# Kernel tuning notes

Measured on AMD Instinct MI355X. Metric: run time of the kernel, lower is better.

The kernel has to match this reference:

```python
import jax, jax.numpy as jnp
import numpy as np

B, N, T, F_IN, H, OUT = 64, 207, 48, 6, 64, 1
RANK = 24  # fixed inner dim of learned adjacency factors


def setup_inputs() -> dict:
    key = jax.random.key(0)
    ks = jax.random.split(key, 10)
    s = lambda k, shp, sc=1.0: jax.random.normal(k, shp, jnp.float32) * sc
    return {
        "x": s(ks[0], (B, N, T, F_IN)),
        "N1": s(ks[1], (N, RANK)),
        "N2": s(ks[2], (RANK, N)),
        "W1": s(ks[3], (F_IN, H), 0.2),
        "b1": jnp.zeros((H,), jnp.float32),
        "W2": s(ks[4], (H, H), 0.1),
        "b2": jnp.zeros((H,), jnp.float32),
        "W_ih": s(ks[5], (4 * H, H), 0.1),
        "W_hh": s(ks[6], (4 * H, H), 0.1),
        "b_ih": jnp.zeros((4 * H,), jnp.float32),
        "b_hh": jnp.zeros((4 * H,), jnp.float32),
        "W_fc": s(ks[7], (H, OUT), 0.1),
        "b_fc": jnp.zeros((OUT,), jnp.float32),
    }


def reference(x, N1, N2, W1, b1, W2, b2, W_ih, W_hh, b_ih, b_hh, W_fc, b_fc):
    Bn, Nn, Tn, Fn = x.shape
    # sigmoid(N1@N2) > 0 everywhere -> dense_to_sparse yields ALL N^2 edges
    # (self-loops included); GCNConv's gcn_norm adds one extra self-loop,
    # edge weights all 1 -> A = ones + I, deg = N+1, symmetric normalization.
    adj = jax.nn.sigmoid(N1 @ N2)
    mask = (adj > 0).astype(x.dtype)  # structurally all-ones
    A = mask + jnp.eye(Nn, dtype=x.dtype)
    dinv = jax.lax.rsqrt(A.sum(axis=1))
    A_hat = dinv[:, None] * A * dinv[None, :]  # [N, N]

    xt = jnp.transpose(x, (0, 2, 1, 3))  # [B, T, N, F]
    # GCNConv: propagate(x @ W) with sym-norm, then bias; relu; dropout=eval no-op
    h = jax.nn.relu(jnp.einsum('mn,btnh->btmh', A_hat, xt @ W1) + b1)
    h = jax.nn.relu(jnp.einsum('mn,btnh->btmh', A_hat, h @ W2) + b2)

    # [B, T, N, H] -> [B*N, T, H] for the LSTM
    seq = jnp.transpose(h, (0, 2, 1, 3)).reshape(Bn * Nn, Tn, -1)
    Hd = W_hh.shape[1]

    def step(carry, x_t):
        h_prev, c_prev = carry
        g = x_t @ W_ih.T + b_ih + h_prev @ W_hh.T + b_hh
        i, f, gg, o = jnp.split(g, 4, axis=-1)  # torch gate order i,f,g,o
        c = jax.nn.sigmoid(f) * c_prev + jax.nn.sigmoid(i) * jnp.tanh(gg)
        h_new = jax.nn.sigmoid(o) * jnp.tanh(c)
        return (h_new, c), None

    h0 = jnp.zeros((Bn * Nn, Hd), x.dtype)
    (hT, _), _ = jax.lax.scan(step, (h0, h0), jnp.transpose(seq, (1, 0, 2)))
    out = hT @ W_fc + b_fc  # [B*N, OUT]
    return out.reshape(Bn, Nn, -1)
```

## Files before the change

kernel.cpp:

```cpp
#include <hip/hip_runtime.h>
#include <math.h>

#define NB 64
#define NN 207
#define NT 48
#define NF 6
#define NH 64
#define NSEQ (NB*NN)
#define NG   (NSEQ/16)
#define TSTRIDE ((size_t)NSEQ*NH)

typedef short bf8_t __attribute__((ext_vector_type(8)));
typedef float f4_t  __attribute__((ext_vector_type(4)));
typedef unsigned short ushort;
typedef unsigned int uint;

__device__ __forceinline__ ushort bf16h(float x){
  uint u = __float_as_uint(x);
  return (ushort)((u + 0x7FFF + ((u>>16)&1)) >> 16);
}
__device__ __forceinline__ float bf16f(ushort h){
  return __uint_as_float((uint)h << 16);
}
__device__ __forceinline__ float fsig(float x){
  return __builtin_amdgcn_rcpf(1.0f + __expf(-x));
}
__device__ __forceinline__ float ftanh(float x){
  x = fminf(15.0f, fmaxf(-15.0f, x));
  float e = __expf(2.0f*x);
  return 1.0f - 2.0f*__builtin_amdgcn_rcpf(e + 1.0f);
}


#define HW 72
#define XS4 28
#define GCN6_LDS_BYTES (208*HW*2 + (207*XS4 + NF*64 + 64 + 64 + 256 + 256 + 32)*4)

__global__ __launch_bounds__(256, 2) void gcn_kernel(
    const float* __restrict__ x, const float* __restrict__ W1, const float* __restrict__ b1,
    const float* __restrict__ W2, const float* __restrict__ b2, uint* __restrict__ sxp)
{
  extern __shared__ char smraw[];
  ushort* h1b = (ushort*)smraw;
  float*  xs4 = (float*)(h1b + 208*HW);
  float*  W1s = xs4 + 207*XS4;
  float*  b1s = W1s + NF*64;
  float*  b2s = b1s + 64;
  float*  S2_ = b2s + 64;
  float*  r1_ = S2_ + 256;
  float*  xsA = r1_ + 256;

  const int tid = threadIdx.x;
  const int tg = blockIdx.x, b = blockIdx.y;
  const float inv = 1.0f/208.0f;
  const int l = tid & 63;
  const int w = __builtin_amdgcn_readfirstlane(tid >> 6);
  const int col = l & 15, q = l >> 4;
  const int cw = w*16 + col;

  S2_[tid] = 0.f;
  r1_[tid] = 0.f;
  if (tid < 32) xsA[tid] = 0.f;
  if (tid < 72) h1b[207*HW + tid] = 0;

  for (int i=tid;i<NF*64;i+=256) W1s[i]=W1[i];
  if (tid<64){ b1s[tid]=b1[tid]; b2s[tid]=b2[tid]; }
  {
    const float* xb = x + (size_t)b*NN*(NT*NF) + (size_t)tg*24;
    for (int i=tid; i<207*6; i+=256){
      int n = i/6, c = (i - n*6)*4;
      *(float4*)&xs4[n*XS4 + c] = *(const float4*)&xb[(size_t)n*(NT*NF) + c];
    }
  }
  __syncthreads();

  if (tid < 192){
    int tt = tid/48, rem = tid - tt*48, f = rem>>3, p = rem&7;
    float ps = 0.f;
    for (int n=p; n<NN; n+=8) ps += xs4[n*XS4 + tt*6 + f];
    atomicAdd(&xsA[tt*8+f], ps);
  }

  float wtmp[16];
  #pragma unroll
  for (int kc=0;kc<2;kc++)
    #pragma unroll
    for (int j=0;j<8;j++)
      wtmp[kc*8+j] = W2[(size_t)(kc*32 + q*8 + j)*64 + cw];
  bf8_t B2[2];
  #pragma unroll
  for (int kc=0;kc<2;kc++){
    bf8_t ph;
    #pragma unroll
    for (int j=0;j<8;j++) ph[j] = (short)bf16h(wtmp[kc*8+j]);
    B2[kc]=ph;
  }
  __syncthreads();

  const int ht4 = (tid & 15) * 4;
  const int nti = tid >> 4;

  #pragma unroll 1
  for (int tt=0; tt<4; tt++){
    const int t = tg*4 + tt;
    {
      float s1v[4];
      #pragma unroll
      for (int j=0;j<4;j++){
        float a = 0.f;
        #pragma unroll
        for (int f=0;f<NF;f++) a += xsA[tt*8+f]*W1s[f*64 + ht4 + j];
        s1v[j] = a;
      }
      float cs0=0.f, cs1=0.f, cs2=0.f, cs3=0.f;
      #pragma unroll 1
      for (int p=0;p<4;p++){
        int nt = p*16 + nti;
        if (nt < 52){
          #pragma unroll
          for (int i=0;i<4;i++){
            int n = 4*nt+i;
            if (n < NN){
              float a0=0.f,a1=0.f,a2=0.f,a3=0.f;
              #pragma unroll
              for (int f=0;f<NF;f++){
                float xv = xs4[n*XS4 + tt*6 + f];
                float4 wv = *(const float4*)&W1s[f*64 + ht4];
                a0+=xv*wv.x; a1+=xv*wv.y; a2+=xv*wv.z; a3+=xv*wv.w;
              }
              float v0=(a0+s1v[0])*inv + b1s[ht4+0]; v0 = v0>0.f?v0:0.f;
              float v1=(a1+s1v[1])*inv + b1s[ht4+1]; v1 = v1>0.f?v1:0.f;
              float v2=(a2+s1v[2])*inv + b1s[ht4+2]; v2 = v2>0.f?v2:0.f;
              float v3=(a3+s1v[3])*inv + b1s[ht4+3]; v3 = v3>0.f?v3:0.f;
              ushort4 hi;
              hi.x=bf16h(v0); hi.y=bf16h(v1); hi.z=bf16h(v2); hi.w=bf16h(v3);
              *(ushort4*)&h1b[n*HW + ht4] = hi;
              cs0+=v0; cs1+=v1; cs2+=v2; cs3+=v3;
            }
          }
        }
      }
      atomicAdd(&r1_[tt*64+ht4+0], cs0);
      atomicAdd(&r1_[tt*64+ht4+1], cs1);
      atomicAdd(&r1_[tt*64+ht4+2], cs2);
      atomicAdd(&r1_[tt*64+ht4+3], cs3);
    }
    __syncthreads();

    {
      int h = tid & 63, pp = tid >> 6;
      float ps = 0.f;
      #pragma unroll
      for (int k=0;k<16;k++) ps += r1_[tt*64+pp*16+k]*W2[(size_t)(pp*16+k)*64 + h];
      atomicAdd(&S2_[tt*64+h], ps);
    }

    f4_t acc[13];
    #pragma unroll
    for (int mt=0;mt<13;mt++){ f4_t z; z[0]=0.f;z[1]=0.f;z[2]=0.f;z[3]=0.f; acc[mt]=z; }
    #pragma unroll 2
    for (int mt=0;mt<13;mt++){
      #pragma unroll
      for (int kc=0;kc<2;kc++){
        bf8_t ah = *(const bf8_t*)(h1b + (mt*16+col)*HW + kc*32 + q*8);
        acc[mt] = __builtin_amdgcn_mfma_f32_16x16x32_bf16(ah, B2[kc], acc[mt], 0,0,0);
      }
    }
    __syncthreads();

    {
      const float s2v = S2_[tt*64+cw], b2v = b2s[cw];
      uint* obase = sxp + ((size_t)t*NSEQ + (size_t)b*NN)*NH + cw;
      #pragma unroll
      for (int mt=0;mt<13;mt++){
        #pragma unroll
        for (int r=0;r<4;r++){
          int n = mt*16 + q*4 + r;
          if (n < NN){
            float v = (acc[mt][r] + s2v)*inv + b2v;
            v = v>0.f ? v : 0.f;
            ushort hb = bf16h(v);
            ushort lb = bf16h(v - bf16f(hb));
            obase[(size_t)n*NH] = ((uint)hb<<16) | (uint)lb;
          }
        }
      }
    }
  }
}

#define HS 68

__global__ __launch_bounds__(256, 1) void lstm8_kernel(
    const uint* __restrict__ sxp,
    const float* __restrict__ Wih, const float* __restrict__ Whh,
    const float* __restrict__ bih, const float* __restrict__ bhh,
    const float* __restrict__ Wfc, const float* __restrict__ bfc, float* __restrict__ out)
{
  __shared__ uint hf[2][16*HS + 4];

  const int tid = threadIdx.x;
  const int l = tid & 63;
  const int w = __builtin_amdgcn_readfirstlane(tid >> 6);
  const int col = l & 15, q = l >> 4;
  const int g = blockIdx.x;

  bf8_t Bh[4][4], Bl[4][4];
  #pragma unroll
  for (int mat=0; mat<2; mat++){
    const float* W = mat ? Whh : Wih;
    #pragma unroll
    for (int ty=0; ty<4; ty++){
      #pragma unroll
      for (int kk=0; kk<2; kk++){
        const float* wp = W + (size_t)(ty*64 + w*16 + col)*64 + kk*32 + q*8;
        bf8_t ph, pl;
        #pragma unroll
        for (int j=0;j<8;j++){
          float wv = wp[j];
          ushort hb = bf16h(wv);
          ph[j] = (short)hb;
          pl[j] = (short)bf16h(wv - bf16f(hb));
        }
        Bh[ty][mat*2+kk] = ph;
        Bl[ty][mat*2+kk] = pl;
      }
    }
  }
  float bias[4];
  #pragma unroll
  for (int ty=0;ty<4;ty++){
    int r = ty*64 + w*16 + col;
    bias[ty] = bih[r] + bhh[r];
  }
  float c[4];
  #pragma unroll
  for (int i=0;i<4;i++) c[i]=0.f;

  for (int i=tid; i<16*HS; i+=256) hf[0][i] = 0;

  const uint* xg = sxp + (size_t)g*1024 + (size_t)(col*64 + q*8);
  uint4 cA0, cA1, cB0, cB1;
  cA0 = *(const uint4*)(xg);
  cA1 = *(const uint4*)(xg + 4);
  cB0 = *(const uint4*)(xg + 32);
  cB1 = *(const uint4*)(xg + 36);

  const int d = w*16 + col;
  const uint* hrd = &hf[0][0] + col*HS + q*8;
  __syncthreads();

  #pragma unroll 2
  for (int t=0; t<NT; t++){
    const int cur = t & 1;
    bf8_t xh[2], xl[2];
    {
      uint u[8];
      u[0]=cA0.x;u[1]=cA0.y;u[2]=cA0.z;u[3]=cA0.w;u[4]=cA1.x;u[5]=cA1.y;u[6]=cA1.z;u[7]=cA1.w;
      #pragma unroll
      for (int j=0;j<8;j++){ xh[0][j]=(short)(u[j]>>16); xl[0][j]=(short)(u[j]&0xffff); }
      u[0]=cB0.x;u[1]=cB0.y;u[2]=cB0.z;u[3]=cB0.w;u[4]=cB1.x;u[5]=cB1.y;u[6]=cB1.z;u[7]=cB1.w;
      #pragma unroll
      for (int j=0;j<8;j++){ xh[1][j]=(short)(u[j]>>16); xl[1][j]=(short)(u[j]&0xffff); }
    }
    if (t+1 < NT){
      const uint* xn = xg + (size_t)(t+1)*TSTRIDE;
      cA0 = *(const uint4*)(xn);
      cA1 = *(const uint4*)(xn + 4);
      cB0 = *(const uint4*)(xn + 32);
      cB1 = *(const uint4*)(xn + 36);
    }
    bf8_t hh[2], hl[2];
    {
      const uint* hb = hrd + (cur ? (16*HS+4) : 0);
      uint4 h0 = *(const uint4*)(hb);
      uint4 h1 = *(const uint4*)(hb + 4);
      uint4 h2 = *(const uint4*)(hb + 32);
      uint4 h3 = *(const uint4*)(hb + 36);
      uint u[8];
      u[0]=h0.x;u[1]=h0.y;u[2]=h0.z;u[3]=h0.w;u[4]=h1.x;u[5]=h1.y;u[6]=h1.z;u[7]=h1.w;
      #pragma unroll
      for (int j=0;j<8;j++){ hh[0][j]=(short)(u[j]>>16); hl[0][j]=(short)(u[j]&0xffff); }
      u[0]=h2.x;u[1]=h2.y;u[2]=h2.z;u[3]=h2.w;u[4]=h3.x;u[5]=h3.y;u[6]=h3.z;u[7]=h3.w;
      #pragma unroll
      for (int j=0;j<8;j++){ hh[1][j]=(short)(u[j]>>16); hl[1][j]=(short)(u[j]&0xffff); }
    }

    f4_t acc[4];
    #pragma unroll
    for (int ty=0;ty<4;ty++){ f4_t z; z[0]=bias[ty];z[1]=bias[ty];z[2]=bias[ty];z[3]=bias[ty]; acc[ty]=z; }
    #pragma unroll
    for (int kk=0;kk<2;kk++){
      #pragma unroll
      for (int ty=0;ty<4;ty++){
        acc[ty] = __builtin_amdgcn_mfma_f32_16x16x32_bf16(xh[kk], Bh[ty][kk],   acc[ty], 0,0,0);
        acc[ty] = __builtin_amdgcn_mfma_f32_16x16x32_bf16(xl[kk], Bh[ty][kk],   acc[ty], 0,0,0);
        acc[ty] = __builtin_amdgcn_mfma_f32_16x16x32_bf16(xh[kk], Bl[ty][kk],   acc[ty], 0,0,0);
        acc[ty] = __builtin_amdgcn_mfma_f32_16x16x32_bf16(hh[kk], Bh[ty][2+kk], acc[ty], 0,0,0);
        acc[ty] = __builtin_amdgcn_mfma_f32_16x16x32_bf16(hl[kk], Bh[ty][2+kk], acc[ty], 0,0,0);
        acc[ty] = __builtin_amdgcn_mfma_f32_16x16x32_bf16(hh[kk], Bl[ty][2+kk], acc[ty], 0,0,0);
      }
    }

    {
      uint* hw = &hf[cur^1][0];
      #pragma unroll
      for (int r=0;r<4;r++){
        float ig = fsig(acc[0][r]);
        float fg = fsig(acc[1][r]);
        float gt = ftanh(acc[2][r]);
        float og = fsig(acc[3][r]);
        float cc = fg*c[r] + ig*gt;
        c[r] = cc;
        float hv = og*ftanh(cc);
        int off = (q*4+r)*HS + d;
        if (t != NT-1){
          ushort hb2 = bf16h(hv);
          ushort lb2 = bf16h(hv - bf16f(hb2));
          hw[off] = ((uint)hb2<<16) | (uint)lb2;
        } else {
          hw[off] = __float_as_uint(hv);
        }
      }
    }
    __syncthreads();
  }

  if (tid < 16){
    float a = bfc[0];
    const uint* hT = &hf[NT&1][0];
    #pragma unroll 8
    for (int k=0;k<64;k++) a += __uint_as_float(hT[tid*HS + k]) * Wfc[k];
    out[g*16 + tid] = a;
  }
}

extern "C" void kernel_launch(void* const* d_in, const int* in_sizes, int n_in,
                              void* d_out, int out_size, void* d_ws, size_t ws_size,
                              hipStream_t stream) {
  const float* x   = (const float*)d_in[0];
  const float* W1  = (const float*)d_in[3];
  const float* b1  = (const float*)d_in[4];
  const float* W2  = (const float*)d_in[5];
  const float* b2  = (const float*)d_in[6];
  const float* Wih = (const float*)d_in[7];
  const float* Whh = (const float*)d_in[8];
  const float* bih = (const float*)d_in[9];
  const float* bhh = (const float*)d_in[10];
  const float* Wfc = (const float*)d_in[11];
  const float* bfc = (const float*)d_in[12];

  uint*  sxp = (uint*)d_ws;
  float* out = (float*)d_out;

  hipFuncSetAttribute((const void*)gcn_kernel, hipFuncAttributeMaxDynamicSharedMemorySize, GCN6_LDS_BYTES);

  gcn_kernel<<<dim3(NT/4, NB), 256, GCN6_LDS_BYTES, stream>>>(x, W1, b1, W2, b2, sxp);
  lstm8_kernel<<<NG, 256, 0, stream>>>(sxp, Wih, Whh, bih, bhh, Wfc, bfc, out);
}
```

Measured before the change: 356.5 us.

## Split LSTM gate work across 8 waves with an LDS gate exchange

The LSTM kernel goes from 256 to 512 threads per block, so each wave computes two 16-row gate tiles instead of four. This halves the MFMA chain per wave on the serial recurrence. Gate preactivations now go through a shared G buffer, and elementwise cell updates are spread over all threads. The next x timestep is staged into LDS through a per-thread uint2 prefetch. In exchange, each step needs two barriers instead of one, plus extra LDS round-trips, which may offset the shorter critical path.

After: 382.3 us. 1.07x slower.

```diff
diff --git a/kernel.cpp b/kernel.cpp
--- a/kernel.cpp
+++ b/kernel.cpp
@@ -189,31 +189,36 @@
   }
 }
 
-#define HS 68
-
-__global__ __launch_bounds__(256, 1) void lstm8_kernel(
+#define GS 20
+
+__global__ __launch_bounds__(512, 2) void lstm9_kernel(
     const uint* __restrict__ sxp,
     const float* __restrict__ Wih, const float* __restrict__ Whh,
     const float* __restrict__ bih, const float* __restrict__ bhh,
     const float* __restrict__ Wfc, const float* __restrict__ bfc, float* __restrict__ out)
 {
-  __shared__ uint hf[2][16*HS + 4];
+  __shared__ float G[256*GS];
+  __shared__ uint hbuf[16*68];
+  __shared__ uint xbuf[16*68];
 
   const int tid = threadIdx.x;
   const int l = tid & 63;
   const int w = __builtin_amdgcn_readfirstlane(tid >> 6);
   const int col = l & 15, q = l >> 4;
-  const int g = blockIdx.x;
-
-  bf8_t Bh[4][4], Bl[4][4];
+  const int blk = blockIdx.x;
+  const int g0 = (2*w)*16 + col;
+  const int g1 = g0 + 16;
+
+  bf8_t Bh[2][4], Bl[2][4];
   #pragma unroll
   for (int mat=0; mat<2; mat++){
     const float* W = mat ? Whh : Wih;
     #pragma unroll
-    for (int ty=0; ty<4; ty++){
+    for (int ti=0; ti<2; ti++){
+      const int row = g0 + ti*16;
       #pragma unroll
       for (int kk=0; kk<2; kk++){
-        const float* wp = W + (size_t)(ty*64 + w*16 + col)*64 + kk*32 + q*8;
+        const float* wp = W + (size_t)row*64 + kk*32 + q*8;
         bf8_t ph, pl;
         #pragma unroll
         for (int j=0;j<8;j++){
@@ -222,116 +227,113 @@
           ph[j] = (short)hb;
           pl[j] = (short)bf16h(wv - bf16f(hb));
         }
-        Bh[ty][mat*2+kk] = ph;
-        Bl[ty][mat*2+kk] = pl;
-      }
-    }
-  }
-  float bias[4];
-  #pragma unroll
-  for (int ty=0;ty<4;ty++){
-    int r = ty*64 + w*16 + col;
-    bias[ty] = bih[r] + bhh[r];
-  }
-  float c[4];
-  #pragma unroll
-  for (int i=0;i<4;i++) c[i]=0.f;
-
-  for (int i=tid; i<16*HS; i+=256) hf[0][i] = 0;
-
-  const uint* xg = sxp + (size_t)g*1024 + (size_t)(col*64 + q*8);
-  uint4 cA0, cA1, cB0, cB1;
-  cA0 = *(const uint4*)(xg);
-  cA1 = *(const uint4*)(xg + 4);
-  cB0 = *(const uint4*)(xg + 32);
-  cB1 = *(const uint4*)(xg + 36);
-
-  const int d = w*16 + col;
-  const uint* hrd = &hf[0][0] + col*HS + q*8;
+        Bh[ti][mat*2+kk] = ph;
+        Bl[ti][mat*2+kk] = pl;
+      }
+    }
+  }
+  const float bias0 = bih[g0] + bhh[g0];
+  const float bias1 = bih[g1] + bhh[g1];
+
+  const int s_p = tid & 15;
+  const int d0p = tid >> 4;
+  float c0 = 0.f, c1 = 0.f;
+
+  for (int i=tid; i<16*68; i+=512) hbuf[i] = 0;
+  {
+    const uint2 px = *(const uint2*)(sxp + (size_t)blk*1024 + tid*2);
+    const int s = (tid*2)>>6, dd = (tid*2)&63;
+    *(uint2*)&xbuf[s*68 + dd] = px;
+  }
+  const int abase = col*68;
   __syncthreads();
 
-  #pragma unroll 2
+  #pragma unroll 1
   for (int t=0; t<NT; t++){
-    const int cur = t & 1;
-    bf8_t xh[2], xl[2];
+    uint2 px;
+    const bool pf = (t+1 < NT);
+    if (pf) px = *(const uint2*)(sxp + (size_t)(t+1)*TSTRIDE + (size_t)blk*1024 + tid*2);
+
+    f4_t acc0, acc1;
+    acc0[0]=bias0; acc0[1]=bias0; acc0[2]=bias0; acc0[3]=bias0;
+    acc1[0]=bias1; acc1[1]=bias1; acc1[2]=bias1; acc1[3]=bias1;
+
+    #pragma unroll
+    for (int kk=0; kk<2; kk++){
+      const uint* xp = &xbuf[abase + kk*32 + q*8];
+      uint4 a = *(const uint4*)xp, b = *(const uint4*)(xp+4);
+      bf8_t xh, xl;
+      uint u[8];
+      u[0]=a.x;u[1]=a.y;u[2]=a.z;u[3]=a.w;u[4]=b.x;u[5]=b.y;u[6]=b.z;u[7]=b.w;
+      #pragma unroll
+      for (int j=0;j<8;j++){ xh[j]=(short)(u[j]>>16); xl[j]=(short)(u[j]&0xffff); }
+      acc0 = __builtin_amdgcn_mfma_f32_16x16x32_bf16(xh, Bh[0][kk], acc0, 0,0,0);
+      acc0 = __builtin_amdgcn_mfma_f32_16x16x32_bf16(xl, Bh[0][kk], acc0, 0,0,0);
+      acc0 = __builtin_amdgcn_mfma_f32_16x16x32_bf16(xh, Bl[0][kk], acc0, 0,0,0);
+      acc1 = __builtin_amdgcn_mfma_f32_16x16x32_bf16(xh, Bh[1][kk], acc1, 0,0,0);
+      acc1 = __builtin_amdgcn_mfma_f32_16x16x32_bf16(xl, Bh[1][kk], acc1, 0,0,0);
+      acc1 = __builtin_amdgcn_mfma_f32_16x16x32_bf16(xh, Bl[1][kk], acc1, 0,0,0);
+    }
+    #pragma unroll
+    for (int kk=0; kk<2; kk++){
+      const uint* hp = &hbuf[abase + kk*32 + q*8];
+      uint4 a = *(const uint4*)hp, b = *(const uint4*)(hp+4);
+      bf8_t hh, hl;
+      uint u[8];
+      u[0]=a.x;u[1]=a.y;u[2]=a.z;u[3]=a.w;u[4]=b.x;u[5]=b.y;u[6]=b.z;u[7]=b.w;
+      #pragma unroll
+      for (int j=0;j<8;j++){ hh[j]=(short)(u[j]>>16); hl[j]=(short)(u[j]&0xffff); }
+      acc0 = __builtin_amdgcn_mfma_f32_16x16x32_bf16(hh, Bh[0][2+kk], acc0, 0,0,0);
+      acc0 = __builtin_amdgcn_mfma_f32_16x16x32_bf16(hl, Bh[0][2+kk], acc0, 0,0,0);
+      acc0 = __builtin_amdgcn_mfma_f32_16x16x32_bf16(hh, Bl[0][2+kk], acc0, 0,0,0);
+      acc1 = __builtin_amdgcn_mfma_f32_16x16x32_bf16(hh, Bh[1][2+kk], acc1, 0,0,0);
+      acc1 = __builtin_amdgcn_mfma_f32_16x16x32_bf16(hl, Bh[1][2+kk], acc1, 0,0,0);
+      acc1 = __builtin_amdgcn_mfma_f32_16x16x32_bf16(hh, Bl[1][2+kk], acc1, 0,0,0);
+    }
+    *(f4_t*)&G[g0*GS + q*4] = acc0;
+    *(f4_t*)&G[g1*GS + q*4] = acc1;
+    __syncthreads();
+
     {
-      uint u[8];
-      u[0]=cA0.x;u[1]=cA0.y;u[2]=cA0.z;u[3]=cA0.w;u[4]=cA1.x;u[5]=cA1.y;u[6]=cA1.z;u[7]=cA1.w;
-      #pragma unroll
-      for (int j=0;j<8;j++){ xh[0][j]=(short)(u[j]>>16); xl[0][j]=(short)(u[j]&0xffff); }
-      u[0]=cB0.x;u[1]=cB0.y;u[2]=cB0.z;u[3]=cB0.w;u[4]=cB1.x;u[5]=cB1.y;u[6]=cB1.z;u[7]=cB1.w;
-      #pragma unroll
-      for (int j=0;j<8;j++){ xh[1][j]=(short)(u[j]>>16); xl[1][j]=(short)(u[j]&0xffff); }
-    }
-    if (t+1 < NT){
-      const uint* xn = xg + (size_t)(t+1)*TSTRIDE;
-      cA0 = *(const uint4*)(xn);
-      cA1 = *(const uint4*)(xn + 4);
-      cB0 = *(const uint4*)(xn + 32);
-      cB1 = *(const uint4*)(xn + 36);
-    }
-    bf8_t hh[2], hl[2];
-    {
-      const uint* hb = hrd + (cur ? (16*HS+4) : 0);
-      uint4 h0 = *(const uint4*)(hb);
-      uint4 h1 = *(const uint4*)(hb + 4);
-      uint4 h2 = *(const uint4*)(hb + 32);
-      uint4 h3 = *(const uint4*)(hb + 36);
-      uint u[8];
-      u[0]=h0.x;u[1]=h0.y;u[2]=h0.z;u[3]=h0.w;u[4]=h1.x;u[5]=h1.y;u[6]=h1.z;u[7]=h1.w;
-      #pragma unroll
-      for (int j=0;j<8;j++){ hh[0][j]=(short)(u[j]>>16); hl[0][j]=(short)(u[j]&0xffff); }
-      u[0]=h2.x;u[1]=h2.y;u[2]=h2.z;u[3]=h2.w;u[4]=h3.x;u[5]=h3.y;u[6]=h3.z;u[7]=h3.w;
-      #pragma unroll
-      for (int j=0;j<8;j++){ hh[1][j]=(short)(u[j]>>16); hl[1][j]=(short)(u[j]&0xffff); }
-    }
-
-    f4_t acc[4];
-    #pragma unroll
-    for (int ty=0;ty<4;ty++){ f4_t z; z[0]=bias[ty];z[1]=bias[ty];z[2]=bias[ty];z[3]=bias[ty]; acc[ty]=z; }
-    #pragma unroll
-    for (int kk=0;kk<2;kk++){
-      #pragma unroll
-      for (int ty=0;ty<4;ty++){
-        acc[ty] = __builtin_amdgcn_mfma_f32_16x16x32_bf16(xh[kk], Bh[ty][kk],   acc[ty], 0,0,0);
-        acc[ty] = __builtin_amdgcn_mfma_f32_16x16x32_bf16(xl[kk], Bh[ty][kk],   acc[ty], 0,0,0);
-        acc[ty] = __builtin_amdgcn_mfma_f32_16x16x32_bf16(xh[kk], Bl[ty][kk],   acc[ty], 0,0,0);
-        acc[ty] = __builtin_amdgcn_mfma_f32_16x16x32_bf16(hh[kk], Bh[ty][2+kk], acc[ty], 0,0,0);
-        acc[ty] = __builtin_amdgcn_mfma_f32_16x16x32_bf16(hl[kk], Bh[ty][2+kk], acc[ty], 0,0,0);
-        acc[ty] = __builtin_amdgcn_mfma_f32_16x16x32_bf16(hh[kk], Bl[ty][2+kk], acc[ty], 0,0,0);
-      }
-    }
-
-    {
-      uint* hw = &hf[cur^1][0];
-      #pragma unroll
-      for (int r=0;r<4;r++){
-        float ig = fsig(acc[0][r]);
-        float fg = fsig(acc[1][r]);
-        float gt = ftanh(acc[2][r]);
-        float og = fsig(acc[3][r]);
-        float cc = fg*c[r] + ig*gt;
-        c[r] = cc;
-        float hv = og*ftanh(cc);
-        int off = (q*4+r)*HS + d;
-        if (t != NT-1){
-          ushort hb2 = bf16h(hv);
-          ushort lb2 = bf16h(hv - bf16f(hb2));
-          hw[off] = ((uint)hb2<<16) | (uint)lb2;
-        } else {
-          hw[off] = __float_as_uint(hv);
-        }
-      }
+      float gi = G[(d0p     )*GS + s_p];
+      float gf = G[(d0p+  64)*GS + s_p];
+      float gg = G[(d0p+ 128)*GS + s_p];
+      float go = G[(d0p+ 192)*GS + s_p];
+      float cc0 = fsig(gf)*c0 + fsig(gi)*ftanh(gg);
+      c0 = cc0;
+      float hv0 = fsig(go)*ftanh(cc0);
+
+      const int d1p = d0p + 32;
+      gi = G[(d1p     )*GS + s_p];
+      gf = G[(d1p+  64)*GS + s_p];
+      gg = G[(d1p+ 128)*GS + s_p];
+      go = G[(d1p+ 192)*GS + s_p];
+      float cc1 = fsig(gf)*c1 + fsig(gi)*ftanh(gg);
+      c1 = cc1;
+      float hv1 = fsig(go)*ftanh(cc1);
+
+      if (t != NT-1){
+        ushort hb0 = bf16h(hv0);
+        hbuf[s_p*68 + d0p] = ((uint)hb0<<16) | (uint)bf16h(hv0 - bf16f(hb0));
+        ushort hb1 = bf16h(hv1);
+        hbuf[s_p*68 + d1p] = ((uint)hb1<<16) | (uint)bf16h(hv1 - bf16f(hb1));
+      } else {
+        hbuf[s_p*68 + d0p] = __float_as_uint(hv0);
+        hbuf[s_p*68 + d1p] = __float_as_uint(hv1);
+      }
+    }
+    if (pf){
+      const int s = (tid*2)>>6, dd = (tid*2)&63;
+      *(uint2*)&xbuf[s*68 + dd] = px;
     }
     __syncthreads();
   }
 
   if (tid < 16){
     float a = bfc[0];
-    const uint* hT = &hf[NT&1][0];
     #pragma unroll 8
-    for (int k=0;k<64;k++) a += __uint_as_float(hT[tid*HS + k]) * Wfc[k];
-    out[g*16 + tid] = a;
+    for (int k=0;k<64;k++) a += __uint_as_float(hbuf[tid*68 + k]) * Wfc[k];
+    out[blk*16 + tid] = a;
   }
 }
 
@@ -356,5 +358,5 @@
   hipFuncSetAttribute((const void*)gcn_kernel, hipFuncAttributeMaxDynamicSharedMemorySize, GCN6_LDS_BYTES);
 
   gcn_kernel<<<dim3(NT/4, NB), 256, GCN6_LDS_BYTES, stream>>>(x, W1, b1, W2, b2, sxp);
-  lstm8_kernel<<<NG, 256, 0, stream>>>(sxp, Wih, Whh, bih, bhh, Wfc, bfc, out);
-}
+  lstm9_kernel<<<NG, 512, 0, stream>>>(sxp, Wih, Whh, bih, bhh, Wfc, bfc, out);
+}
```

## Restructure LSTM kernel to 32-sequence blocks with 32x32x16 MFMA transposed layout

Applied to the files above, without the earlier changes.

Rewrites the LSTM recurrence so each 512-thread block handles 32 sequences instead of 16. It uses 32x32x16 bf16 MFMAs with the weights as the A operand and interleaves gate rows so each lane holds all four gates of a hidden unit. Input and hidden contributions go to separate accumulators so the x-part MFMAs do not depend on the hidden state. This halves the grid and changes the data layout, with more registers per thread and launch bounds of 2 blocks per CU.

Result: slower. 440.2 us (+23.5%).

```diff
diff --git a/kernel.cpp b/kernel.cpp
--- a/kernel.cpp
+++ b/kernel.cpp
@@ -7,11 +7,12 @@
 #define NF 6
 #define NH 64
 #define NSEQ (NB*NN)
-#define NG   (NSEQ/16)
+#define NG32 (NSEQ/32)
 #define TSTRIDE ((size_t)NSEQ*NH)
 
 typedef short bf8_t __attribute__((ext_vector_type(8)));
 typedef float f4_t  __attribute__((ext_vector_type(4)));
+typedef float f16v  __attribute__((ext_vector_type(16)));
 typedef unsigned short ushort;
 typedef unsigned int uint;
 
@@ -189,149 +190,138 @@
   }
 }
 
-#define HS 68
-
-__global__ __launch_bounds__(256, 1) void lstm8_kernel(
+#define HS3 68
+
+__global__ __launch_bounds__(512, 2) void lstm10_kernel(
     const uint* __restrict__ sxp,
     const float* __restrict__ Wih, const float* __restrict__ Whh,
     const float* __restrict__ bih, const float* __restrict__ bhh,
     const float* __restrict__ Wfc, const float* __restrict__ bfc, float* __restrict__ out)
 {
-  __shared__ uint hf[2][16*HS + 4];
+  __shared__ uint hbuf[2][32*HS3];
 
   const int tid = threadIdx.x;
   const int l = tid & 63;
   const int w = __builtin_amdgcn_readfirstlane(tid >> 6);
-  const int col = l & 15, q = l >> 4;
-  const int g = blockIdx.x;
-
-  bf8_t Bh[4][4], Bl[4][4];
-  #pragma unroll
-  for (int mat=0; mat<2; mat++){
-    const float* W = mat ? Whh : Wih;
-    #pragma unroll
-    for (int ty=0; ty<4; ty++){
-      #pragma unroll
-      for (int kk=0; kk<2; kk++){
-        const float* wp = W + (size_t)(ty*64 + w*16 + col)*64 + kk*32 + q*8;
-        bf8_t ph, pl;
-        #pragma unroll
-        for (int j=0;j<8;j++){
-          float wv = wp[j];
-          ushort hb = bf16h(wv);
-          ph[j] = (short)hb;
-          pl[j] = (short)bf16h(wv - bf16f(hb));
-        }
-        Bh[ty][mat*2+kk] = ph;
-        Bl[ty][mat*2+kk] = pl;
-      }
-    }
-  }
-  float bias[4];
-  #pragma unroll
-  for (int ty=0;ty<4;ty++){
-    int r = ty*64 + w*16 + col;
-    bias[ty] = bih[r] + bhh[r];
+  const int sl = l & 31;
+  const int half = l >> 5;
+  const int blk = blockIdx.x;
+  const int s0 = blk*32;
+
+  const int orow = (sl&3)*64 + w*8 + ((sl>>2)&7);
+  bf8_t Ah[8], Al[8];
+  #pragma unroll
+  for (int kc=0;kc<8;kc++){
+    const float* W = (kc<4) ? Wih : Whh;
+    const float* wp = W + (size_t)orow*64 + (kc&3)*16 + half*8;
+    bf8_t ph, pl;
+    #pragma unroll
+    for (int j=0;j<8;j++){
+      float wv = wp[j];
+      ushort hb = bf16h(wv);
+      ph[j] = (short)hb;
+      pl[j] = (short)bf16h(wv - bf16f(hb));
+    }
+    Ah[kc]=ph; Al[kc]=pl;
+  }
+  float bias[16];
+  #pragma unroll
+  for (int m4=0;m4<4;m4++){
+    const int d = 8*w + 2*m4 + half;
+    #pragma unroll
+    for (int ty=0;ty<4;ty++) bias[4*m4+ty] = bih[ty*64+d] + bhh[ty*64+d];
   }
   float c[4];
   #pragma unroll
   for (int i=0;i<4;i++) c[i]=0.f;
 
-  for (int i=tid; i<16*HS; i+=256) hf[0][i] = 0;
-
-  const uint* xg = sxp + (size_t)g*1024 + (size_t)(col*64 + q*8);
-  uint4 cA0, cA1, cB0, cB1;
-  cA0 = *(const uint4*)(xg);
-  cA1 = *(const uint4*)(xg + 4);
-  cB0 = *(const uint4*)(xg + 32);
-  cB1 = *(const uint4*)(xg + 36);
-
-  const int d = w*16 + col;
-  const uint* hrd = &hf[0][0] + col*HS + q*8;
+  for (int i=tid;i<32*HS3;i+=512) hbuf[0][i]=0;
+
+  const uint* xg = sxp + ((size_t)s0 + sl)*64 + half*8;
+  uint4 px[8];
+  #pragma unroll
+  for (int kb=0;kb<4;kb++){
+    px[kb*2  ] = *(const uint4*)(xg + kb*16);
+    px[kb*2+1] = *(const uint4*)(xg + kb*16 + 4);
+  }
+  const int hrd = sl*HS3 + half*8;
   __syncthreads();
 
-  #pragma unroll 2
+  #pragma unroll 1
   for (int t=0; t<NT; t++){
     const int cur = t & 1;
-    bf8_t xh[2], xl[2];
+    uint4 nx[8];
+    const bool pf = (t+1 < NT);
+    if (pf){
+      const uint* xn = xg + (size_t)(t+1)*TSTRIDE;
+      #pragma unroll
+      for (int kb=0;kb<4;kb++){
+        nx[kb*2  ] = *(const uint4*)(xn + kb*16);
+        nx[kb*2+1] = *(const uint4*)(xn + kb*16 + 4);
+      }
+    }
+
+    f16v accx, acch;
+    #pragma unroll
+    for (int i=0;i<16;i++){ accx[i]=bias[i]; acch[i]=0.f; }
+
+    #pragma unroll
+    for (int kb=0;kb<4;kb++){
+      uint u[8];
+      uint4 a = px[kb*2], b = px[kb*2+1];
+      u[0]=a.x;u[1]=a.y;u[2]=a.z;u[3]=a.w;u[4]=b.x;u[5]=b.y;u[6]=b.z;u[7]=b.w;
+      bf8_t xh, xl;
+      #pragma unroll
+      for (int j=0;j<8;j++){ xh[j]=(short)(u[j]>>16); xl[j]=(short)(u[j]&0xffff); }
+      accx = __builtin_amdgcn_mfma_f32_32x32x16_bf16(Ah[kb], xh, accx, 0,0,0);
+      accx = __builtin_amdgcn_mfma_f32_32x32x16_bf16(Al[kb], xh, accx, 0,0,0);
+      accx = __builtin_amdgcn_mfma_f32_32x32x16_bf16(Ah[kb], xl, accx, 0,0,0);
+    }
+    #pragma unroll
+    for (int kb=0;kb<4;kb++){
+      const uint* hp = &hbuf[cur][hrd + kb*16];
+      uint4 a = *(const uint4*)hp, b = *(const uint4*)(hp+4);
+      uint u[8];
+      u[0]=a.x;u[1]=a.y;u[2]=a.z;u[3]=a.w;u[4]=b.x;u[5]=b.y;u[6]=b.z;u[7]=b.w;
+      bf8_t hh, hl;
+      #pragma unroll
+      for (int j=0;j<8;j++){ hh[j]=(short)(u[j]>>16); hl[j]=(short)(u[j]&0xffff); }
+      acch = __builtin_amdgcn_mfma_f32_32x32x16_bf16(Ah[4+kb], hh, acch, 0,0,0);
+      acch = __builtin_amdgcn_mfma_f32_32x32x16_bf16(Al[4+kb], hh, acch, 0,0,0);
+      acch = __builtin_amdgcn_mfma_f32_32x32x16_bf16(Ah[4+kb], hl, acch, 0,0,0);
+    }
+
     {
-      uint u[8];
-      u[0]=cA0.x;u[1]=cA0.y;u[2]=cA0.z;u[3]=cA0.w;u[4]=cA1.x;u[5]=cA1.y;u[6]=cA1.z;u[7]=cA1.w;
-      #pragma unroll
-      for (int j=0;j<8;j++){ xh[0][j]=(short)(u[j]>>16); xl[0][j]=(short)(u[j]&0xffff); }
-      u[0]=cB0.x;u[1]=cB0.y;u[2]=cB0.z;u[3]=cB0.w;u[4]=cB1.x;u[5]=cB1.y;u[6]=cB1.z;u[7]=cB1.w;
-      #pragma unroll
-      for (int j=0;j<8;j++){ xh[1][j]=(short)(u[j]>>16); xl[1][j]=(short)(u[j]&0xffff); }
-    }
-    if (t+1 < NT){
-      const uint* xn = xg + (size_t)(t+1)*TSTRIDE;
-      cA0 = *(const uint4*)(xn);
-      cA1 = *(const uint4*)(xn + 4);
-      cB0 = *(const uint4*)(xn + 32);
-      cB1 = *(const uint4*)(xn + 36);
-    }
-    bf8_t hh[2], hl[2];
-    {
-      const uint* hb = hrd + (cur ? (16*HS+4) : 0);
-      uint4 h0 = *(const uint4*)(hb);
-      uint4 h1 = *(const uint4*)(hb + 4);
-      uint4 h2 = *(const uint4*)(hb + 32);
-      uint4 h3 = *(const uint4*)(hb + 36);
-      uint u[8];
-      u[0]=h0.x;u[1]=h0.y;u[2]=h0.z;u[3]=h0.w;u[4]=h1.x;u[5]=h1.y;u[6]=h1.z;u[7]=h1.w;
-      #pragma unroll
-      for (int j=0;j<8;j++){ hh[0][j]=(short)(u[j]>>16); hl[0][j]=(short)(u[j]&0xffff); }
-      u[0]=h2.x;u[1]=h2.y;u[2]=h2.z;u[3]=h2.w;u[4]=h3.x;u[5]=h3.y;u[6]=h3.z;u[7]=h3.w;
-      #pragma unroll
-      for (int j=0;j<8;j++){ hh[1][j]=(short)(u[j]>>16); hl[1][j]=(short)(u[j]&0xffff); }
-    }
-
-    f4_t acc[4];
-    #pragma unroll
-    for (int ty=0;ty<4;ty++){ f4_t z; z[0]=bias[ty];z[1]=bias[ty];z[2]=bias[ty];z[3]=bias[ty]; acc[ty]=z; }
-    #pragma unroll
-    for (int kk=0;kk<2;kk++){
-      #pragma unroll
-      for (int ty=0;ty<4;ty++){
-        acc[ty] = __builtin_amdgcn_mfma_f32_16x16x32_bf16(xh[kk], Bh[ty][kk],   acc[ty], 0,0,0);
-        acc[ty] = __builtin_amdgcn_mfma_f32_16x16x32_bf16(xl[kk], Bh[ty][kk],   acc[ty], 0,0,0);
-        acc[ty] = __builtin_amdgcn_mfma_f32_16x16x32_bf16(xh[kk], Bl[ty][kk],   acc[ty], 0,0,0);
-        acc[ty] = __builtin_amdgcn_mfma_f32_16x16x32_bf16(hh[kk], Bh[ty][2+kk], acc[ty], 0,0,0);
-        acc[ty] = __builtin_amdgcn_mfma_f32_16x16x32_bf16(hl[kk], Bh[ty][2+kk], acc[ty], 0,0,0);
-        acc[ty] = __builtin_amdgcn_mfma_f32_16x16x32_bf16(hh[kk], Bl[ty][2+kk], acc[ty], 0,0,0);
-      }
-    }
-
-    {
-      uint* hw = &hf[cur^1][0];
-      #pragma unroll
-      for (int r=0;r<4;r++){
-        float ig = fsig(acc[0][r]);
-        float fg = fsig(acc[1][r]);
-        float gt = ftanh(acc[2][r]);
-        float og = fsig(acc[3][r]);
-        float cc = fg*c[r] + ig*gt;
-        c[r] = cc;
-        float hv = og*ftanh(cc);
-        int off = (q*4+r)*HS + d;
+      uint* hw_ = &hbuf[cur^1][0];
+      #pragma unroll
+      for (int m4=0;m4<4;m4++){
+        float gi = accx[4*m4+0] + acch[4*m4+0];
+        float gf = accx[4*m4+1] + acch[4*m4+1];
+        float gg = accx[4*m4+2] + acch[4*m4+2];
+        float go = accx[4*m4+3] + acch[4*m4+3];
+        float cc = fsig(gf)*c[m4] + fsig(gi)*ftanh(gg);
+        c[m4] = cc;
+        float hv = fsig(go)*ftanh(cc);
+        const int d = 8*w + 2*m4 + half;
         if (t != NT-1){
           ushort hb2 = bf16h(hv);
-          ushort lb2 = bf16h(hv - bf16f(hb2));
-          hw[off] = ((uint)hb2<<16) | (uint)lb2;
+          hw_[sl*HS3 + d] = ((uint)hb2<<16) | (uint)bf16h(hv - bf16f(hb2));
         } else {
-          hw[off] = __float_as_uint(hv);
+          hw_[sl*HS3 + d] = __float_as_uint(hv);
         }
       }
     }
+    #pragma unroll
+    for (int i=0;i<8;i++) px[i] = nx[i];
     __syncthreads();
   }
 
-  if (tid < 16){
+  if (tid < 32){
     float a = bfc[0];
-    const uint* hT = &hf[NT&1][0];
+    const uint* hT = &hbuf[NT & 1][0];
     #pragma unroll 8
-    for (int k=0;k<64;k++) a += __uint_as_float(hT[tid*HS + k]) * Wfc[k];
-    out[g*16 + tid] = a;
+    for (int k=0;k<64;k++) a += __uint_as_float(hT[tid*HS3 + k]) * Wfc[k];
+    out[s0 + tid] = a;
   }
 }
 
@@ -356,5 +346,5 @@
   hipFuncSetAttribute((const void*)gcn_kernel, hipFuncAttributeMaxDynamicSharedMemorySize, GCN6_LDS_BYTES);
 
   gcn_kernel<<<dim3(NT/4, NB), 256, GCN6_LDS_BYTES, stream>>>(x, W1, b1, W2, b2, sxp);
-  lstm8_kernel<<<NG, 256, 0, stream>>>(sxp, Wih, Whh, bih, bhh, Wfc, bfc, out);
-}
+  lstm10_kernel<<<NG32, 512, 0, stream>>>(sxp, Wih, Whh, bih, bhh, Wfc, bfc, out);
+}
```

## Split bf16 hi/lo activations into separate planes and widen GCN time tile

Applied to the files above, without the earlier changes.

The intermediate sequence buffer and the LSTM hidden-state LDS buffer are stored as two separate bf16 planes (hi and lo) instead of packed 32-bit words. The LSTM can then load MFMA operands directly as bf16x8 vectors, with no per-step shift and mask unpacking. The GCN kernel now handles 6 timesteps per block instead of 4, which gives fewer blocks and amortizes the per-block setup, at the cost of more LDS. The split-plane global writes are 16-bit scattered stores, which may coalesce less well than the packed 32-bit stores.

Result: slower. 386.0 us (+8.3%).

```diff
diff --git a/kernel.cpp b/kernel.cpp
--- a/kernel.cpp
+++ b/kernel.cpp
@@ -8,7 +8,7 @@
 #define NH 64
 #define NSEQ (NB*NN)
 #define NG   (NSEQ/16)
-#define TSTRIDE ((size_t)NSEQ*NH)
+#define TSU  ((size_t)NSEQ*NH)
 
 typedef short bf8_t __attribute__((ext_vector_type(8)));
 typedef float f4_t  __attribute__((ext_vector_type(4)));
@@ -33,22 +33,23 @@
 
 
 #define HW 72
-#define XS4 28
-#define GCN6_LDS_BYTES (208*HW*2 + (207*XS4 + NF*64 + 64 + 64 + 256 + 256 + 32)*4)
+#define XS6 40
+#define GCN7_LDS_BYTES (208*HW*2 + (207*XS6 + NF*64 + 64 + 64 + 6*64 + 6*64 + 48)*4)
 
 __global__ __launch_bounds__(256, 2) void gcn_kernel(
     const float* __restrict__ x, const float* __restrict__ W1, const float* __restrict__ b1,
-    const float* __restrict__ W2, const float* __restrict__ b2, uint* __restrict__ sxp)
+    const float* __restrict__ W2, const float* __restrict__ b2,
+    ushort* __restrict__ sxh, ushort* __restrict__ sxl)
 {
   extern __shared__ char smraw[];
   ushort* h1b = (ushort*)smraw;
-  float*  xs4 = (float*)(h1b + 208*HW);
-  float*  W1s = xs4 + 207*XS4;
+  float*  xs6 = (float*)(h1b + 208*HW);
+  float*  W1s = xs6 + 207*XS6;
   float*  b1s = W1s + NF*64;
   float*  b2s = b1s + 64;
   float*  S2_ = b2s + 64;
-  float*  r1_ = S2_ + 256;
-  float*  xsA = r1_ + 256;
+  float*  r1_ = S2_ + 6*64;
+  float*  xsA = r1_ + 6*64;
 
   const int tid = threadIdx.x;
   const int tg = blockIdx.x, b = blockIdx.y;
@@ -58,26 +59,25 @@
   const int col = l & 15, q = l >> 4;
   const int cw = w*16 + col;
 
-  S2_[tid] = 0.f;
-  r1_[tid] = 0.f;
-  if (tid < 32) xsA[tid] = 0.f;
+  for (int i=tid; i<6*64; i+=256){ S2_[i]=0.f; r1_[i]=0.f; }
+  if (tid < 48) xsA[tid] = 0.f;
   if (tid < 72) h1b[207*HW + tid] = 0;
 
   for (int i=tid;i<NF*64;i+=256) W1s[i]=W1[i];
   if (tid<64){ b1s[tid]=b1[tid]; b2s[tid]=b2[tid]; }
   {
-    const float* xb = x + (size_t)b*NN*(NT*NF) + (size_t)tg*24;
-    for (int i=tid; i<207*6; i+=256){
-      int n = i/6, c = (i - n*6)*4;
-      *(float4*)&xs4[n*XS4 + c] = *(const float4*)&xb[(size_t)n*(NT*NF) + c];
+    const float* xb = x + (size_t)b*NN*(NT*NF) + (size_t)tg*36;
+    for (int i=tid; i<207*9; i+=256){
+      int n = i/9, c = (i - n*9)*4;
+      *(float4*)&xs6[n*XS6 + c] = *(const float4*)&xb[(size_t)n*(NT*NF) + c];
     }
   }
   __syncthreads();
 
-  if (tid < 192){
-    int tt = tid/48, rem = tid - tt*48, f = rem>>3, p = rem&7;
+  if (tid < 144){
+    int tt = tid/24, rem = tid - tt*24, f = rem>>2, p = rem&3;
     float ps = 0.f;
-    for (int n=p; n<NN; n+=8) ps += xs4[n*XS4 + tt*6 + f];
+    for (int n=p; n<NN; n+=4) ps += xs6[n*XS6 + tt*6 + f];
     atomicAdd(&xsA[tt*8+f], ps);
   }
 
@@ -101,8 +101,8 @@
   const int nti = tid >> 4;
 
   #pragma unroll 1
-  for (int tt=0; tt<4; tt++){
-    const int t = tg*4 + tt;
+  for (int tt=0; tt<6; tt++){
+    const int t = tg*6 + tt;
     {
       float s1v[4];
       #pragma unroll
@@ -124,7 +124,7 @@
               float a0=0.f,a1=0.f,a2=0.f,a3=0.f;
               #pragma unroll
               for (int f=0;f<NF;f++){
-                float xv = xs4[n*XS4 + tt*6 + f];
+                float xv = xs6[n*XS6 + tt*6 + f];
                 float4 wv = *(const float4*)&W1s[f*64 + ht4];
                 a0+=xv*wv.x; a1+=xv*wv.y; a2+=xv*wv.z; a3+=xv*wv.w;
               }
@@ -170,7 +170,7 @@
 
     {
       const float s2v = S2_[tt*64+cw], b2v = b2s[cw];
-      uint* obase = sxp + ((size_t)t*NSEQ + (size_t)b*NN)*NH + cw;
+      const size_t obase = (size_t)t*TSU + (size_t)(b*NN)*NH + cw;
       #pragma unroll
       for (int mt=0;mt<13;mt++){
         #pragma unroll
@@ -180,8 +180,8 @@
             float v = (acc[mt][r] + s2v)*inv + b2v;
             v = v>0.f ? v : 0.f;
             ushort hb = bf16h(v);
-            ushort lb = bf16h(v - bf16f(hb));
-            obase[(size_t)n*NH] = ((uint)hb<<16) | (uint)lb;
+            sxh[obase + (size_t)n*NH] = hb;
+            sxl[obase + (size_t)n*NH] = bf16h(v - bf16f(hb));
           }
         }
       }
@@ -189,15 +189,16 @@
   }
 }
 
-#define HS 68
-
-__global__ __launch_bounds__(256, 1) void lstm8_kernel(
-    const uint* __restrict__ sxp,
+#define HS2 72
+
+__global__ __launch_bounds__(256, 1) void lstm11_kernel(
+    const ushort* __restrict__ sxh, const ushort* __restrict__ sxl,
     const float* __restrict__ Wih, const float* __restrict__ Whh,
     const float* __restrict__ bih, const float* __restrict__ bhh,
     const float* __restrict__ Wfc, const float* __restrict__ bfc, float* __restrict__ out)
 {
-  __shared__ uint hf[2][16*HS + 4];
+  __shared__ ushort hhp[2][16*HS2];
+  __shared__ ushort hlp[2][16*HS2];
 
   const int tid = threadIdx.x;
   const int l = tid & 63;
@@ -237,73 +238,57 @@
   #pragma unroll
   for (int i=0;i<4;i++) c[i]=0.f;
 
-  for (int i=tid; i<16*HS; i+=256) hf[0][i] = 0;
-
-  const uint* xg = sxp + (size_t)g*1024 + (size_t)(col*64 + q*8);
-  uint4 cA0, cA1, cB0, cB1;
-  cA0 = *(const uint4*)(xg);
-  cA1 = *(const uint4*)(xg + 4);
-  cB0 = *(const uint4*)(xg + 32);
-  cB1 = *(const uint4*)(xg + 36);
+  for (int i=tid; i<16*HS2; i+=256){ hhp[0][i]=0; hlp[0][i]=0; }
+
+  const ushort* xgh = sxh + (size_t)g*1024 + (size_t)(col*64 + q*8);
+  const ushort* xgl = sxl + (size_t)g*1024 + (size_t)(col*64 + q*8);
+  bf8_t cxh[2], cxl[2];
+  cxh[0] = *(const bf8_t*)(xgh);
+  cxh[1] = *(const bf8_t*)(xgh + 32);
+  cxl[0] = *(const bf8_t*)(xgl);
+  cxl[1] = *(const bf8_t*)(xgl + 32);
 
   const int d = w*16 + col;
-  const uint* hrd = &hf[0][0] + col*HS + q*8;
+  const int hro = col*HS2 + q*8;
   __syncthreads();
 
   #pragma unroll 2
   for (int t=0; t<NT; t++){
     const int cur = t & 1;
-    bf8_t xh[2], xl[2];
+    bf8_t nxh[2], nxl[2];
+    const bool pf = (t+1 < NT);
+    if (pf){
+      const size_t off = (size_t)(t+1)*TSU;
+      nxh[0] = *(const bf8_t*)(xgh + off);
+      nxh[1] = *(const bf8_t*)(xgh + off + 32);
+      nxl[0] = *(const bf8_t*)(xgl + off);
+      nxl[1] = *(const bf8_t*)(xgl + off + 32);
+    }
+    bf8_t hh[2], hl[2];
+    hh[0] = *(const bf8_t*)&hhp[cur][hro];
+    hh[1] = *(const bf8_t*)&hhp[cur][hro + 32];
+    hl[0] = *(const bf8_t*)&hlp[cur][hro];
+    hl[1] = *(const bf8_t*)&hlp[cur][hro + 32];
+
+    f4_t acc[4];
+    #pragma unroll
+    for (int ty=0;ty<4;ty++){ f4_t z; z[0]=bias[ty];z[1]=bias[ty];z[2]=bias[ty];z[3]=bias[ty]; acc[ty]=z; }
+    #pragma unroll
+    for (int kk=0;kk<2;kk++){
+      #pragma unroll
+      for (int ty=0;ty<4;ty++){
+        acc[ty] = __builtin_amdgcn_mfma_f32_16x16x32_bf16(cxh[kk], Bh[ty][kk],   acc[ty], 0,0,0);
+        acc[ty] = __builtin_amdgcn_mfma_f32_16x16x32_bf16(cxl[kk], Bh[ty][kk],   acc[ty], 0,0,0);
+        acc[ty] = __builtin_amdgcn_mfma_f32_16x16x32_bf16(cxh[kk], Bl[ty][kk],   acc[ty], 0,0,0);
+        acc[ty] = __builtin_amdgcn_mfma_f32_16x16x32_bf16(hh[kk],  Bh[ty][2+kk], acc[ty], 0,0,0);
+        acc[ty] = __builtin_amdgcn_mfma_f32_16x16x32_bf16(hl[kk],  Bh[ty][2+kk], acc[ty], 0,0,0);
+        acc[ty] = __builtin_amdgcn_mfma_f32_16x16x32_bf16(hh[kk],  Bl[ty][2+kk], acc[ty], 0,0,0);
+      }
+    }
+
     {
-      uint u[8];
-      u[0]=cA0.x;u[1]=cA0.y;u[2]=cA0.z;u[3]=cA0.w;u[4]=cA1.x;u[5]=cA1.y;u[6]=cA1.z;u[7]=cA1.w;
-      #pragma unroll
-      for (int j=0;j<8;j++){ xh[0][j]=(short)(u[j]>>16); xl[0][j]=(short)(u[j]&0xffff); }
-      u[0]=cB0.x;u[1]=cB0.y;u[2]=cB0.z;u[3]=cB0.w;u[4]=cB1.x;u[5]=cB1.y;u[6]=cB1.z;u[7]=cB1.w;
-      #pragma unroll
-      for (int j=0;j<8;j++){ xh[1][j]=(short)(u[j]>>16); xl[1][j]=(short)(u[j]&0xffff); }
-    }
-    if (t+1 < NT){
-      const uint* xn = xg + (size_t)(t+1)*TSTRIDE;
-      cA0 = *(const uint4*)(xn);
-      cA1 = *(const uint4*)(xn + 4);
-      cB0 = *(const uint4*)(xn + 32);
-      cB1 = *(const uint4*)(xn + 36);
-    }
-    bf8_t hh[2], hl[2];
-    {
-      const uint* hb = hrd + (cur ? (16*HS+4) : 0);
-      uint4 h0 = *(const uint4*)(hb);
-      uint4 h1 = *(const uint4*)(hb + 4);
-      uint4 h2 = *(const uint4*)(hb + 32);
-      uint4 h3 = *(const uint4*)(hb + 36);
-      uint u[8];
-      u[0]=h0.x;u[1]=h0.y;u[2]=h0.z;u[3]=h0.w;u[4]=h1.x;u[5]=h1.y;u[6]=h1.z;u[7]=h1.w;
-      #pragma unroll
-      for (int j=0;j<8;j++){ hh[0][j]=(short)(u[j]>>16); hl[0][j]=(short)(u[j]&0xffff); }
-      u[0]=h2.x;u[1]=h2.y;u[2]=h2.z;u[3]=h2.w;u[4]=h3.x;u[5]=h3.y;u[6]=h3.z;u[7]=h3.w;
-      #pragma unroll
-      for (int j=0;j<8;j++){ hh[1][j]=(short)(u[j]>>16); hl[1][j]=(short)(u[j]&0xffff); }
-    }
-
-    f4_t acc[4];
-    #pragma unroll
-    for (int ty=0;ty<4;ty++){ f4_t z; z[0]=bias[ty];z[1]=bias[ty];z[2]=bias[ty];z[3]=bias[ty]; acc[ty]=z; }
-    #pragma unroll
-    for (int kk=0;kk<2;kk++){
-      #pragma unroll
-      for (int ty=0;ty<4;ty++){
-        acc[ty] = __builtin_amdgcn_mfma_f32_16x16x32_bf16(xh[kk], Bh[ty][kk],   acc[ty], 0,0,0);
-        acc[ty] = __builtin_amdgcn_mfma_f32_16x16x32_bf16(xl[kk], Bh[ty][kk],   acc[ty], 0,0,0);
-        acc[ty] = __builtin_amdgcn_mfma_f32_16x16x32_bf16(xh[kk], Bl[ty][kk],   acc[ty], 0,0,0);
-        acc[ty] = __builtin_amdgcn_mfma_f32_16x16x32_bf16(hh[kk], Bh[ty][2+kk], acc[ty], 0,0,0);
-        acc[ty] = __builtin_amdgcn_mfma_f32_16x16x32_bf16(hl[kk], Bh[ty][2+kk], acc[ty], 0,0,0);
-        acc[ty] = __builtin_amdgcn_mfma_f32_16x16x32_bf16(hh[kk], Bl[ty][2+kk], acc[ty], 0,0,0);
-      }
-    }
-
-    {
-      uint* hw = &hf[cur^1][0];
+      ushort* hwh = &hhp[cur^1][0];
+      ushort* hwl = &hlp[cur^1][0];
       #pragma unroll
       for (int r=0;r<4;r++){
         float ig = fsig(acc[0][r]);
@@ -313,24 +298,30 @@
         float cc = fg*c[r] + ig*gt;
         c[r] = cc;
         float hv = og*ftanh(cc);
-        int off = (q*4+r)*HS + d;
+        int off = (q*4+r)*HS2 + d;
         if (t != NT-1){
           ushort hb2 = bf16h(hv);
-          ushort lb2 = bf16h(hv - bf16f(hb2));
-          hw[off] = ((uint)hb2<<16) | (uint)lb2;
+          hwh[off] = hb2;
+          hwl[off] = bf16h(hv - bf16f(hb2));
         } else {
-          hw[off] = __float_as_uint(hv);
+          uint bits = __float_as_uint(hv);
+          hwh[off] = (ushort)(bits >> 16);
+          hwl[off] = (ushort)(bits & 0xffff);
         }
       }
     }
+    #pragma unroll
+    for (int kk=0;kk<2;kk++){ cxh[kk]=nxh[kk]; cxl[kk]=nxl[kk]; }
     __syncthreads();
   }
 
   if (tid < 16){
     float a = bfc[0];
-    const uint* hT = &hf[NT&1][0];
     #pragma unroll 8
-    for (int k=0;k<64;k++) a += __uint_as_float(hT[tid*HS + k]) * Wfc[k];
+    for (int k=0;k<64;k++){
+      uint bits = ((uint)hhp[0][tid*HS2 + k] << 16) | (uint)hlp[0][tid*HS2 + k];
+      a += __uint_as_float(bits) * Wfc[k];
+    }
     out[g*16 + tid] = a;
   }
 }
@@ -350,11 +341,12 @@
   const float* Wfc = (const float*)d_in[11];
   const float* bfc = (const float*)d_in[12];
 
-  uint*  sxp = (uint*)d_ws;
-  float* out = (float*)d_out;
-
-  hipFuncSetAttribute((const void*)gcn_kernel, hipFuncAttributeMaxDynamicSharedMemorySize, GCN6_LDS_BYTES);
-
-  gcn_kernel<<<dim3(NT/4, NB), 256, GCN6_LDS_BYTES, stream>>>(x, W1, b1, W2, b2, sxp);
-  lstm8_kernel<<<NG, 256, 0, stream>>>(sxp, Wih, Whh, bih, bhh, Wfc, bfc, out);
-}
+  ushort* sxh = (ushort*)d_ws;
+  ushort* sxl = sxh + (size_t)NT*TSU;
+  float*  out = (float*)d_out;
+
+  hipFuncSetAttribute((const void*)gcn_kernel, hipFuncAttributeMaxDynamicSharedMemorySize, GCN7_LDS_BYTES);
+
+  gcn_kernel<<<dim3(NT/6, NB), 256, GCN7_LDS_BYTES, stream>>>(x, W1, b1, W2, b2, sxh, sxl);
+  lstm11_kernel<<<NG, 256, 0, stream>>>(sxh, sxl, Wih, Whh, bih, bhh, Wfc, bfc, out);
+}
```
